# Kernel optimization log

Hardware: AMD Instinct MI355X
Metric: run time of the kernel (lower is better)

The kernel has to match this reference:

```python
import jax, jax.numpy as jnp
import numpy as np

B = 2048
NU, NF, NA = 20000, 100000, 20000  # users, feeds, authors
D = 150   # SVD embed dim for FM features
DK = 64   # tag/keyword/d2v embed dim


def setup_inputs() -> dict:
    key = jax.random.key(0)
    ks = jax.random.split(key, 24)
    r = lambda k, shape: (jax.random.normal(k, shape, dtype=jnp.float32) * 0.05)
    # ids: user, feed, author columns with their own vocab ranges
    u = jax.random.randint(ks[0], (B,), 0, NU)
    f = jax.random.randint(ks[1], (B,), 0, NF)
    a = jax.random.randint(ks[2], (B,), 0, NA)
    inputs = jnp.stack([u, f, a], axis=1).astype(jnp.int32)  # [B,3]
    first_order_shifts = jnp.array([0, NU, NU + NF], dtype=jnp.int32)
    return {
        'inputs': inputs,
        'first_order_shifts': first_order_shifts,
        'W_user_feed': r(ks[3], (NU, D)),
        'W_feed_user': r(ks[4], (NF, D)),
        'W_user_author': r(ks[5], (NU, D)),
        'W_author_user': r(ks[6], (NA, D)),
        'W_feed_emb': r(ks[7], (NF, D)),          # trainable=False in original
        'W_user_tag': r(ks[8], (NU, DK)),
        'W_user_key1': r(ks[9], (NU, DK)),
        'W_user_key2': r(ks[10], (NU, DK)),
        'W_feed_tag': r(ks[11], (NF, DK)),
        'W_feed_key1': r(ks[12], (NF, DK)),
        'W_feed_key2': r(ks[13], (NF, DK)),
        'W_uf_d2v': r(ks[14], (NU, DK)),
        'W_fu_d2v': r(ks[15], (NF, DK)),
        'W_ua_d2v': r(ks[16], (NU, DK)),
        'W_au_d2v': r(ks[17], (NA, DK)),
        'W256': r(ks[18], (2 * D * D, 256)),       # 45000 -> 256
        'b256': jnp.zeros((256,), jnp.float32),
        'W128': r(ks[19], (2 * DK * DK, 128)),     # 8192 -> 128
        'b128': jnp.zeros((128,), jnp.float32),
    }


def reference(inputs, first_order_shifts, W_user_feed, W_feed_user,
              W_user_author, W_author_user, W_feed_emb, W_user_tag,
              W_user_key1, W_user_key2, W_feed_tag, W_feed_key1, W_feed_key2,
              W_uf_d2v, W_fu_d2v, W_ua_d2v, W_au_d2v, W256, b256, W128, b128):
    inputs = inputs.reshape(-1, 3)
    u, f, a = inputs[:, 0], inputs[:, 1], inputs[:, 2]
    one_hot_inputs = inputs + first_order_shifts[None, :]

    user_feed_embed = W_user_feed[u]      # [B,150]
    user_author_embed = W_user_author[u]
    author_user_embed = W_author_user[a]
    feed_emb_embed = W_feed_emb[f]
    feed_user_embed = W_feed_user[f]
    user_tag_embed = W_user_tag[u]        # [B,64]
    user_key1_embed = W_user_key1[u]
    user_key2_embed = W_user_key2[u]
    feed_tag_embed = W_feed_tag[f]
    feed_key1_embed = W_feed_key1[f]
    feed_key2_embed = W_feed_key2[f]
    user_feed_d2vem = W_uf_d2v[u]
    user_author_d2vem = W_ua_d2v[u]
    feed_user_d2vem = W_fu_d2v[f]
    author_user_d2vem = W_au_d2v[a]

    # d2v outer products -> [B,64,64] each; concat axis=1 -> [B,128,64]
    user_w_feed = jnp.einsum('bi,bj->bij', user_feed_d2vem, feed_user_d2vem)
    user_w_auth = jnp.einsum('bi,bj->bij', user_author_d2vem, author_user_d2vem)
    user_w_user = jnp.concatenate([user_w_feed, user_w_auth], axis=1)
    user_w_user = user_w_user.reshape(-1, 2 * DK * DK)
    user_w_user = jax.nn.relu(user_w_user @ W128 + b128)  # Dropout inactive (inference)

    # SVD outer products -> [B,150,150] each; concat axis=1 -> [B,300,150]
    user_x_feed = jnp.einsum('bi,bj->bij', user_feed_embed, feed_user_embed)
    user_x_auth = jnp.einsum('bi,bj->bij', user_author_embed, author_user_embed)
    user_x_user = jnp.concatenate([user_x_feed, user_x_auth], axis=1)
    user_x_user = user_x_user.reshape(-1, 2 * D * D)
    user_x_user = jax.nn.relu(user_x_user @ W256 + b256)

    # tf.concat([list], axis=1) stacks the inner list -> [4,B,150], then reshape (-1,4,150)
    embeds_fm = jnp.stack([user_feed_embed, user_author_embed,
                           feed_user_embed, author_user_embed], axis=0)
    fm_embed_inputs = embeds_fm.reshape(-1, 4, D)

    expert_inputs = jnp.concatenate([
        user_feed_embed, user_author_embed, user_tag_embed, user_key1_embed,
        user_key2_embed, user_feed_d2vem, user_author_d2vem, feed_user_embed,
        feed_tag_embed, feed_key1_embed, feed_emb_embed, feed_key2_embed,
        feed_user_d2vem, author_user_embed, author_user_d2vem,
        user_x_user, user_w_user], axis=-1)  # [B,1710]
    return expert_inputs, one_hot_inputs, fm_embed_inputs
```

## Files before the change

### kernel.cpp

```cpp
#include <hip/hip_runtime.h>
#include <hip/hip_bf16.h>
#include <stdint.h>

#define BB   2048
#define DD   150
#define DKK  64

static constexpr int EXPERT_W  = 1774;
static constexpr int X_OFF     = 1390;
static constexpr int W_OFF     = 1646;
static constexpr int EXPERT_SZ = BB * EXPERT_W;
static constexpr int OH_BASE   = EXPERT_SZ;
static constexpr int FM_BASE   = OH_BASE + BB * 3;

static constexpr size_t WTX_OFF = 0;
static constexpr size_t WTW_OFF = 24576000;
static constexpr size_t WSX_OFF = 26673152;
static constexpr size_t WSW_OFF = 43450368;
static constexpr size_t WS_NEED = 51838976;

typedef __attribute__((ext_vector_type(8))) short bf16x8;
typedef __attribute__((ext_vector_type(4))) float f32x4;

union APack { int d[4]; bf16x8 v; };

__device__ __forceinline__ int cvtpk_bf16(float a, float b) {
  int r; asm("v_cvt_pk_bf16_f32 %0, %1, %2" : "=v"(r) : "v"(a), "v"(b)); return r;
}
__device__ __forceinline__ f32x4 mfma16(bf16x8 a, bf16x8 b, f32x4 c) {
  return __builtin_amdgcn_mfma_f32_16x16x32_bf16(a, b, c, 0, 0, 0);
}
__device__ __forceinline__ void gload16(const void* g, void* l) {
  __builtin_amdgcn_global_load_lds(
      (__attribute__((address_space(1))) void*)(g),
      (__attribute__((address_space(3))) void*)(l), 16, 0, 0);
}
__device__ __forceinline__ float bfu2f(uint32_t u) { return __uint_as_float(u << 16); }

__global__ __launch_bounds__(256) void prep_pack(
    const float* __restrict__ W256, __hip_bfloat16* __restrict__ WtX,
    const float* __restrict__ W128, __hip_bfloat16* __restrict__ WtW)
{
  const int blk = blockIdx.x;
  const int t = threadIdx.x;

  if (blk < 1500) {
    const int T  = blk;
    const int jj = T / 300;
    const int i  = T - jj*300;
    float v[32];
    const float* src = W256 + ((size_t)i*150 + jj*32)*256 + t;
    #pragma unroll
    for (int jl = 0; jl < 32; ++jl) {
      int j = jj*32 + jl;
      v[jl] = (j < 150) ? src[(size_t)jl*256] : 0.f;
    }
    const int b16 = t >> 4, nloc = t & 15;
    char* dst = (char*)WtX + (size_t)T*16384 + (size_t)(b16*512 + nloc*8)*2;
    #pragma unroll
    for (int ksub = 0; ksub < 4; ++ksub) {
      int pk0 = cvtpk_bf16(v[ksub*8+0], v[ksub*8+1]);
      int pk1 = cvtpk_bf16(v[ksub*8+2], v[ksub*8+3]);
      int pk2 = cvtpk_bf16(v[ksub*8+4], v[ksub*8+5]);
      int pk3 = cvtpk_bf16(v[ksub*8+6], v[ksub*8+7]);
      *(int4*)(dst + (size_t)ksub*256) = make_int4(pk0, pk1, pk2, pk3);
    }
  } else {
    if (t >= 128) return;
    const int T  = blk - 1500;
    const int jj = T >> 7;
    const int i  = T & 127;
    float v[32];
    const float* src = W128 + ((size_t)i*64 + jj*32)*128 + t;
    #pragma unroll
    for (int jl = 0; jl < 32; ++jl) v[jl] = src[(size_t)jl*128];
    const int b16 = t >> 4, nloc = t & 15;
    char* dst = (char*)WtW + (size_t)T*8192 + (size_t)(b16*512 + nloc*8)*2;
    #pragma unroll
    for (int ksub = 0; ksub < 4; ++ksub) {
      int pk0 = cvtpk_bf16(v[ksub*8+0], v[ksub*8+1]);
      int pk1 = cvtpk_bf16(v[ksub*8+2], v[ksub*8+3]);
      int pk2 = cvtpk_bf16(v[ksub*8+4], v[ksub*8+5]);
      int pk3 = cvtpk_bf16(v[ksub*8+6], v[ksub*8+7]);
      *(int4*)(dst + (size_t)ksub*256) = make_int4(pk0, pk1, pk2, pk3);
    }
  }
}

__global__ __launch_bounds__(512, 4) void mfma_fused(
    const int* __restrict__ inputs, const int* __restrict__ shifts,
    const float* __restrict__ Wuf, const float* __restrict__ Wua,
    const float* __restrict__ Wfu, const float* __restrict__ Wau,
    const float* __restrict__ Wfe,
    const float* __restrict__ Wut, const float* __restrict__ Wuk1, const float* __restrict__ Wuk2,
    const float* __restrict__ Wft, const float* __restrict__ Wfk1, const float* __restrict__ Wfk2,
    const float* __restrict__ Wufd, const float* __restrict__ Wuad,
    const float* __restrict__ Wfud, const float* __restrict__ Waud,
    const __hip_bfloat16* __restrict__ WtXt, __hip_bfloat16* __restrict__ wsX,
    const __hip_bfloat16* __restrict__ WtWt, __hip_bfloat16* __restrict__ wsW,
    float* __restrict__ out)
{
  __shared__ __align__(16) char smem[43008];
  const int tid = threadIdx.x;
  const int lane = tid & 63;
  const int w  = tid >> 6;
  const int lr = lane & 15;
  const int g  = lane >> 4;
  const unsigned wdst = (unsigned)(tid & ~63) * 16;

  if (blockIdx.x < 512) {
    float* xlds = (float*)smem;
    char*  bbase = smem + 10240;

    const int bid = blockIdx.x;
    const int h  = bid & 1;
    const int s  = (bid >> 1) & 15;
    const int mb = bid >> 5;
    const int b0 = mb * 128;
    const bool upper = s >= 8;
    const int sl  = upper ? s - 8 : s;
    const int i0l = sl * 19;
    const int cnt = (150 - i0l) < 19 ? (150 - i0l) : 19;
    const int ig0 = i0l + (upper ? 150 : 0);

    const float* X = upper ? Wua : Wuf;
    const float* Y = upper ? Wau : Wfu;
    const int yoff = upper ? 2 : 1;

    for (int k = tid; k < 128*20; k += 512) {
      int r = k / 20, ii = k - r*20;
      float v = 0.f;
      if (ii < cnt) v = X[(size_t)inputs[(b0+r)*3]*150 + i0l + ii];
      xlds[k] = v;
    }

    const int mg = w >> 1;
    const int ng = w & 1;

    int yid[2];
    #pragma unroll
    for (int mf = 0; mf < 2; ++mf)
      yid[mf] = inputs[(size_t)(b0 + mg*32 + mf*16 + lr)*3 + yoff];

    const char* wtb = (const char*)WtXt + (size_t)h*8192;

    int jjs = 0, iis = 0;
    auto stage1 = [&](int slot) {
      const char* sp = wtb + (size_t)(jjs*300 + ig0 + iis)*16384 + (size_t)tid*16;
      gload16(sp, bbase + (unsigned)slot*8192 + wdst);
      if (iis + 1 < cnt) ++iis;
      else if (jjs + 1 < 5) { iis = 0; ++jjs; }
    };

    f32x4 acc[2][4];
    #pragma unroll
    for (int i = 0; i < 2; ++i)
      #pragma unroll
      for (int j = 0; j < 4; ++j) acc[i][j] = (f32x4){0.f,0.f,0.f,0.f};

    const int NW = 5 * cnt;

    stage1(0); stage1(1); stage1(2);

    int jjc = 0, iic = 0;
    int yjj = -1;
    float yreg[2][8];

    for (int wi = 0; wi < NW; ++wi) {
      const int ahead = NW - 1 - wi;
      if (ahead >= 2)      asm volatile("s_waitcnt vmcnt(2)" ::: "memory");
      else if (ahead == 1) asm volatile("s_waitcnt vmcnt(1)" ::: "memory");
      else                 asm volatile("s_waitcnt vmcnt(0)" ::: "memory");
      __builtin_amdgcn_s_barrier();

      if (wi + 3 < NW) stage1((wi + 3) & 3);
      __builtin_amdgcn_sched_barrier(0);
      __builtin_amdgcn_s_setprio(1);

      if (jjc != yjj) {
        yjj = jjc;
        const int jb = jjc*32 + g*8;
        #pragma unroll
        for (int mf = 0; mf < 2; ++mf) {
          const float* yp = Y + (size_t)yid[mf]*150;
          if (jb + 8 <= 150) {
            #pragma unroll
            for (int hh = 0; hh < 4; ++hh) {
              float2 vv = *(const float2*)(yp + jb + 2*hh);
              yreg[mf][2*hh]   = vv.x;
              yreg[mf][2*hh+1] = vv.y;
            }
          } else {
            #pragma unroll
            for (int e = 0; e < 8; ++e)
              yreg[mf][e] = (jb + e < 150) ? yp[jb + e] : 0.f;
          }
        }
      }
      const __hip_bfloat16* bb = (const __hip_bfloat16*)(bbase + (unsigned)(wi & 3)*8192);
      bf16x8 bv[4];
      #pragma unroll
      for (int nf = 0; nf < 4; ++nf)
        bv[nf] = *(const bf16x8*)(bb + (ng*4 + nf)*512 + g*128 + lr*8);
      APack a[2];
      #pragma unroll
      for (int mf = 0; mf < 2; ++mf) {
        const float xv = xlds[(mg*32 + mf*16 + lr)*20 + iic];
        #pragma unroll
        for (int e = 0; e < 4; ++e)
          a[mf].d[e] = cvtpk_bf16(xv*yreg[mf][2*e], xv*yreg[mf][2*e+1]);
      }
      #pragma unroll
      for (int mf = 0; mf < 2; ++mf)
        #pragma unroll
        for (int nf = 0; nf < 4; ++nf)
          acc[mf][nf] = mfma16(a[mf].v, bv[nf], acc[mf][nf]);

      __builtin_amdgcn_s_setprio(0);
      ++iic; if (iic >= cnt) { iic = 0; ++jjc; }
    }

    __hip_bfloat16* wp = wsX + ((size_t)s*2048 + b0)*256;
    #pragma unroll
    for (int mf = 0; mf < 2; ++mf) {
      #pragma unroll
      for (int nf = 0; nf < 4; ++nf) {
        int rb  = mg*32 + mf*16 + g*4;
        int col = h*128 + ng*64 + nf*16 + lr;
        f32x4 v = acc[mf][nf];
        #pragma unroll
        for (int e = 0; e < 4; ++e)
          wp[(size_t)(rb+e)*256 + col] = __float2bfloat16(v[e]);
      }
    }

  } else if (blockIdx.x < 768) {
    float* xlds = (float*)smem;
    char*  bbase = smem + 4096;

    const int bidw = blockIdx.x - 512;
    const int mb = bidw >> 4;
    const int s  = bidw & 15;
    const int b0 = mb * 128;
    const bool upper = s >= 8;
    const int i0l = (s & 7) * 8;
    const int ig0 = i0l + (upper ? 64 : 0);

    const float* X = upper ? Wuad : Wufd;
    const float* Y = upper ? Waud : Wfud;
    const int yoff = upper ? 2 : 1;

    for (int k = tid; k < 128*8; k += 512) {
      int r = k >> 3, ii = k & 7;
      xlds[k] = X[(size_t)inputs[(size_t)(b0+r)*3]*64 + i0l + ii];
    }

    const int mg = w >> 1;
    const int ng = w & 1;

    int yid[2];
    #pragma unroll
    for (int mf = 0; mf < 2; ++mf)
      yid[mf] = inputs[(size_t)(b0 + mg*32 + mf*16 + lr)*3 + yoff];

    const char* wtb = (const char*)WtWt;

    auto stageT = [&](int bufi, int T) {
      const char* sp = wtb + (size_t)T*8192 + (size_t)tid*16;
      char* dp = bbase + (unsigned)bufi*16384 + wdst;
      gload16(sp,        dp);
      gload16(sp + 8192, dp + 8192);
    };

    f32x4 acc[2][4];
    #pragma unroll
    for (int i = 0; i < 2; ++i)
      #pragma unroll
      for (int j = 0; j < 4; ++j) acc[i][j] = (f32x4){0.f,0.f,0.f,0.f};

    stageT(0, ig0);
    stageT(1, ig0 + 2);

    int jjc = 0, iic = 0;
    int jjs = 0, iis = 4;
    int yjj = -1;
    float yreg[2][8];

    for (int p = 0; p < 8; ++p) {
      if (jjc != yjj) {
        yjj = jjc;
        const int jb = jjc*32 + g*8;
        #pragma unroll
        for (int mf = 0; mf < 2; ++mf) {
          const float* yp = Y + (size_t)yid[mf]*64 + jb;
          #pragma unroll
          for (int hh = 0; hh < 2; ++hh) {
            float4 v = *(const float4*)(yp + hh*4);
            yreg[mf][hh*4]   = v.x;
            yreg[mf][hh*4+1] = v.y;
            yreg[mf][hh*4+2] = v.z;
            yreg[mf][hh*4+3] = v.w;
          }
        }
      }
      if (p + 1 < 8) asm volatile("s_waitcnt vmcnt(2)" ::: "memory");
      else           asm volatile("s_waitcnt vmcnt(0)" ::: "memory");
      __builtin_amdgcn_s_barrier();
      __builtin_amdgcn_sched_barrier(0);

      const int buf = p & 1;
      #pragma unroll
      for (int sc = 0; sc < 2; ++sc) {
        const __hip_bfloat16* bb = (const __hip_bfloat16*)(bbase + (unsigned)buf*16384 + (unsigned)sc*8192);
        bf16x8 bv[4];
        #pragma unroll
        for (int nf = 0; nf < 4; ++nf)
          bv[nf] = *(const bf16x8*)(bb + (ng*4 + nf)*512 + g*128 + lr*8);
        APack a[2];
        #pragma unroll
        for (int mf = 0; mf < 2; ++mf) {
          float xv = xlds[(mg*32 + mf*16 + lr)*8 + iic + sc];
          #pragma unroll
          for (int e = 0; e < 4; ++e)
            a[mf].d[e] = cvtpk_bf16(xv*yreg[mf][2*e], xv*yreg[mf][2*e+1]);
        }
        #pragma unroll
        for (int mf = 0; mf < 2; ++mf)
          #pragma unroll
          for (int nf = 0; nf < 4; ++nf)
            acc[mf][nf] = mfma16(a[mf].v, bv[nf], acc[mf][nf]);
      }

      __builtin_amdgcn_s_barrier();
      if (p + 2 < 8) stageT(buf, jjs*128 + ig0 + iis);

      iic += 2; if (iic >= 8) { iic = 0; ++jjc; }
      iis += 2; if (iis >= 8) { iis = 0; ++jjs; }
    }

    __hip_bfloat16* wp = wsW + ((size_t)s*2048 + b0)*128;
    #pragma unroll
    for (int mf = 0; mf < 2; ++mf) {
      #pragma unroll
      for (int nf = 0; nf < 4; ++nf) {
        int rb  = mg*32 + mf*16 + g*4;
        int col = ng*64 + nf*16 + lr;
        f32x4 v = acc[mf][nf];
        #pragma unroll
        for (int e = 0; e < 4; ++e)
          wp[(size_t)(rb+e)*128 + col] = __float2bfloat16(v[e]);
      }
    }

  } else {
    const int b = blockIdx.x - 768;
    const int u = inputs[b*3 + 0];
    const int f = inputs[b*3 + 1];
    const int a = inputs[b*3 + 2];
    float* row = out + b * EXPERT_W;
    float* fm  = out + FM_BASE;
    const int t = tid;

    for (int c = t; c < DD; c += 512) {
        float ufe = Wuf[u*DD + c];
        float uae = Wua[u*DD + c];
        float fue = Wfu[f*DD + c];
        float fee = Wfe[f*DD + c];
        float aue = Wau[a*DD + c];
        row[0    + c] = ufe;
        row[150  + c] = uae;
        row[620  + c] = fue;
        row[898  + c] = fee;
        row[1176 + c] = aue;
        fm[0*BB*DD + b*DD + c] = ufe;
        fm[1*BB*DD + b*DD + c] = uae;
        fm[2*BB*DD + b*DD + c] = fue;
        fm[3*BB*DD + b*DD + c] = aue;
    }
    for (int c = t; c < DKK; c += 512) {
        row[300  + c] = Wut [u*DKK + c];
        row[364  + c] = Wuk1[u*DKK + c];
        row[428  + c] = Wuk2[u*DKK + c];
        row[492  + c] = Wufd[u*DKK + c];
        row[556  + c] = Wuad[u*DKK + c];
        row[770  + c] = Wft [f*DKK + c];
        row[834  + c] = Wfk1[f*DKK + c];
        row[1048 + c] = Wfk2[f*DKK + c];
        row[1112 + c] = Wfud[f*DKK + c];
        row[1326 + c] = Waud[a*DKK + c];
    }
    if (t < 3) out[OH_BASE + b*3 + t] = (float)(inputs[b*3 + t] + shifts[t]);
  }
}

__global__ __launch_bounds__(256) void epilogue_kernel(
    const __hip_bfloat16* __restrict__ wsX, const __hip_bfloat16* __restrict__ wsW,
    const float* __restrict__ b256, const float* __restrict__ b128,
    float* __restrict__ out)
{
  int idx = blockIdx.x*256 + threadIdx.x;
  if (idx >= BB*192) return;
  int b = idx / 192, c2 = idx - b*192;
  if (c2 < 128) {
    int c = c2*2;
    float a0 = b256[c], a1 = b256[c+1];
    #pragma unroll
    for (int k = 0; k < 16; ++k) {
      uint32_t u = *(const uint32_t*)(wsX + ((size_t)k*BB + b)*256 + c);
      a0 += bfu2f(u);
      a1 += __uint_as_float(u & 0xffff0000u);
    }
    float2 r = make_float2(a0 > 0.f ? a0 : 0.f, a1 > 0.f ? a1 : 0.f);
    *(float2*)(out + (size_t)b*EXPERT_W + X_OFF + c) = r;
  } else {
    int cc = (c2 - 128)*2;
    float a0 = b128[cc], a1 = b128[cc+1];
    #pragma unroll
    for (int k = 0; k < 16; ++k) {
      uint32_t u = *(const uint32_t*)(wsW + ((size_t)k*BB + b)*128 + cc);
      a0 += bfu2f(u);
      a1 += __uint_as_float(u & 0xffff0000u);
    }
    float2 r = make_float2(a0 > 0.f ? a0 : 0.f, a1 > 0.f ? a1 : 0.f);
    *(float2*)(out + (size_t)b*EXPERT_W + W_OFF + cc) = r;
  }
}

__global__ __launch_bounds__(256) void gather_kernel(
    const int* __restrict__ inputs, const int* __restrict__ shifts,
    const float* __restrict__ Wuf, const float* __restrict__ Wfu,
    const float* __restrict__ Wua, const float* __restrict__ Wau,
    const float* __restrict__ Wfe,
    const float* __restrict__ Wut, const float* __restrict__ Wuk1, const float* __restrict__ Wuk2,
    const float* __restrict__ Wft, const float* __restrict__ Wfk1, const float* __restrict__ Wfk2,
    const float* __restrict__ Wufd, const float* __restrict__ Wfud,
    const float* __restrict__ Wuad, const float* __restrict__ Waud,
    float* __restrict__ out)
{
    const int b = blockIdx.x;
    const int u = inputs[b*3 + 0];
    const int f = inputs[b*3 + 1];
    const int a = inputs[b*3 + 2];
    float* row = out + b * EXPERT_W;
    float* fm  = out + FM_BASE;
    const int t = threadIdx.x;

    for (int c = t; c < DD; c += 256) {
        float ufe = Wuf[u*DD + c];
        float uae = Wua[u*DD + c];
        float fue = Wfu[f*DD + c];
        float fee = Wfe[f*DD + c];
        float aue = Wau[a*DD + c];
        row[0    + c] = ufe;
        row[150  + c] = uae;
        row[620  + c] = fue;
        row[898  + c] = fee;
        row[1176 + c] = aue;
        fm[0*BB*DD + b*DD + c] = ufe;
        fm[1*BB*DD + b*DD + c] = uae;
        fm[2*BB*DD + b*DD + c] = fue;
        fm[3*BB*DD + b*DD + c] = aue;
    }
    for (int c = t; c < DKK; c += 256) {
        row[300  + c] = Wut [u*DKK + c];
        row[364  + c] = Wuk1[u*DKK + c];
        row[428  + c] = Wuk2[u*DKK + c];
        row[492  + c] = Wufd[u*DKK + c];
        row[556  + c] = Wuad[u*DKK + c];
        row[770  + c] = Wft [f*DKK + c];
        row[834  + c] = Wfk1[f*DKK + c];
        row[1048 + c] = Wfk2[f*DKK + c];
        row[1112 + c] = Wfud[f*DKK + c];
        row[1326 + c] = Waud[a*DKK + c];
    }
    if (t < 3) {
        out[OH_BASE + b*3 + t] = (float)(inputs[b*3 + t] + shifts[t]);
    }
}

static constexpr int NPAIR_X = 300 * 150;
static constexpr int CHX     = 128;

__global__ __launch_bounds__(256) void xuser_kernel(
    const int* __restrict__ inputs,
    const float* __restrict__ Wuf, const float* __restrict__ Wua,
    const float* __restrict__ Wfu, const float* __restrict__ Wau,
    const float* __restrict__ W256, const float* __restrict__ b256,
    float* __restrict__ out)
{
    __shared__ float xs[16][308];
    __shared__ float ys[16][308];
    __shared__ float xy[CHX][16];
    const int half = blockIdx.x & 1;
    const int bg   = blockIdx.x >> 1;
    const int b0   = bg * 16;
    const int t    = threadIdx.x;
    const int bl   = t & 15;
    const int kg   = t >> 4;
    const int kbase = half * 128 + kg * 8;
    for (int idx = t; idx < 16 * DD; idx += 256) {
        int bb = idx / DD;
        int c  = idx - bb * DD;
        int u = inputs[(b0+bb)*3 + 0];
        int f = inputs[(b0+bb)*3 + 1];
        int a = inputs[(b0+bb)*3 + 2];
        xs[bb][c]       = Wuf[u*DD + c];
        xs[bb][150 + c] = Wua[u*DD + c];
        ys[bb][c]       = Wfu[f*DD + c];
        ys[bb][150 + c] = Wau[a*DD + c];
    }
    float acc[8] = {0,0,0,0,0,0,0,0};
    for (int base = 0; base < NPAIR_X; base += CHX) {
        __syncthreads();
        #pragma unroll
        for (int r = 0; r < (CHX*16)/256; ++r) {
            int idx = t + r * 256;
            int pl  = idx >> 4;
            int bb  = idx & 15;
            int p   = base + pl;
            if (p < NPAIR_X) {
                int i = p / 150;
                int j = p - i * 150;
                xy[pl][bb] = xs[bb][i] * ys[bb][(i >= 150 ? 150 : 0) + j];
            }
        }
        __syncthreads();
        const int lim = min(CHX, NPAIR_X - base);
        const float* wp = W256 + base * 256 + kbase;
        for (int pl = 0; pl < lim; ++pl) {
            float sv = xy[pl][bl];
            const float4* w4 = (const float4*)(wp + pl * 256);
            float4 w0 = w4[0], w1 = w4[1];
            acc[0] = fmaf(sv, w0.x, acc[0]); acc[1] = fmaf(sv, w0.y, acc[1]);
            acc[2] = fmaf(sv, w0.z, acc[2]); acc[3] = fmaf(sv, w0.w, acc[3]);
            acc[4] = fmaf(sv, w1.x, acc[4]); acc[5] = fmaf(sv, w1.y, acc[5]);
            acc[6] = fmaf(sv, w1.z, acc[6]); acc[7] = fmaf(sv, w1.w, acc[7]);
        }
    }
    const int rowbase = (b0 + bl) * EXPERT_W + X_OFF;
    #pragma unroll
    for (int m = 0; m < 8; ++m) {
        float v = acc[m] + b256[kbase + m];
        out[rowbase + kbase + m] = (v > 0.f ? v : 0.f);
    }
}

static constexpr int NPAIR_W = 128 * 64;
static constexpr int CHW     = 256;

__global__ __launch_bounds__(256) void wuser_kernel(
    const int* __restrict__ inputs,
    const float* __restrict__ Wufd, const float* __restrict__ Wuad,
    const float* __restrict__ Wfud, const float* __restrict__ Waud,
    const float* __restrict__ W128, const float* __restrict__ b128,
    float* __restrict__ out)
{
    __shared__ float xs[8][132];
    __shared__ float ys[8][132];
    __shared__ float xy[CHW][8];
    const int bg = blockIdx.x;
    const int b0 = bg * 8;
    const int t  = threadIdx.x;
    const int bl = t & 7;
    const int kg = t >> 3;
    const int kbase = kg * 4;
    for (int idx = t; idx < 8 * DKK; idx += 256) {
        int bb = idx >> 6;
        int c  = idx & 63;
        int u = inputs[(b0+bb)*3 + 0];
        int f = inputs[(b0+bb)*3 + 1];
        int a = inputs[(b0+bb)*3 + 2];
        xs[bb][c]      = Wufd[u*DKK + c];
        xs[bb][64 + c] = Wuad[u*DKK + c];
        ys[bb][c]      = Wfud[f*DKK + c];
        ys[bb][64 + c] = Waud[a*DKK + c];
    }
    float acc[4] = {0,0,0,0};
    for (int base = 0; base < NPAIR_W; base += CHW) {
        __syncthreads();
        #pragma unroll
        for (int r = 0; r < (CHW*8)/256; ++r) {
            int idx = t + r * 256;
            int pl  = idx >> 3;
            int bb  = idx & 7;
            int p   = base + pl;
            int i = p >> 6;
            int j = p & 63;
            xy[pl][bb] = xs[bb][i] * ys[bb][(i >= 64 ? 64 : 0) + j];
        }
        __syncthreads();
        const float* wp = W128 + base * 128 + kbase;
        for (int pl = 0; pl < CHW; ++pl) {
            float sv = xy[pl][bl];
            float4 wv = *(const float4*)(wp + pl * 128);
            acc[0] = fmaf(sv, wv.x, acc[0]); acc[1] = fmaf(sv, wv.y, acc[1]);
            acc[2] = fmaf(sv, wv.z, acc[2]); acc[3] = fmaf(sv, wv.w, acc[3]);
        }
    }
    const int rowbase = (b0 + bl) * EXPERT_W + W_OFF;
    #pragma unroll
    for (int m = 0; m < 4; ++m) {
        float v = acc[m] + b128[kbase + m];
        out[rowbase + kbase + m] = (v > 0.f ? v : 0.f);
    }
}

extern "C" void kernel_launch(void* const* d_in, const int* in_sizes, int n_in,
                              void* d_out, int out_size, void* d_ws, size_t ws_size,
                              hipStream_t stream)
{
    const int*   inputs = (const int*)  d_in[0];
    const int*   shifts = (const int*)  d_in[1];
    const float* Wuf    = (const float*)d_in[2];
    const float* Wfu    = (const float*)d_in[3];
    const float* Wua    = (const float*)d_in[4];
    const float* Wau    = (const float*)d_in[5];
    const float* Wfe    = (const float*)d_in[6];
    const float* Wut    = (const float*)d_in[7];
    const float* Wuk1   = (const float*)d_in[8];
    const float* Wuk2   = (const float*)d_in[9];
    const float* Wft    = (const float*)d_in[10];
    const float* Wfk1   = (const float*)d_in[11];
    const float* Wfk2   = (const float*)d_in[12];
    const float* Wufd   = (const float*)d_in[13];
    const float* Wfud   = (const float*)d_in[14];
    const float* Wuad   = (const float*)d_in[15];
    const float* Waud   = (const float*)d_in[16];
    const float* W256   = (const float*)d_in[17];
    const float* b256   = (const float*)d_in[18];
    const float* W128   = (const float*)d_in[19];
    const float* b128   = (const float*)d_in[20];

    float* out = (float*)d_out;

    if (ws_size >= WS_NEED) {
        char* ws = (char*)d_ws;
        __hip_bfloat16* WtX = (__hip_bfloat16*)(ws + WTX_OFF);
        __hip_bfloat16* WtW = (__hip_bfloat16*)(ws + WTW_OFF);
        __hip_bfloat16* wsX = (__hip_bfloat16*)(ws + WSX_OFF);
        __hip_bfloat16* wsW = (__hip_bfloat16*)(ws + WSW_OFF);

        prep_pack<<<1756, 256, 0, stream>>>(W256, WtX, W128, WtW);

        mfma_fused<<<2816, 512, 0, stream>>>(inputs, shifts,
            Wuf, Wua, Wfu, Wau, Wfe, Wut, Wuk1, Wuk2, Wft, Wfk1, Wfk2,
            Wufd, Wuad, Wfud, Waud,
            WtX, wsX, WtW, wsW, out);

        epilogue_kernel<<<(BB*192 + 255)/256, 256, 0, stream>>>(wsX, wsW, b256, b128, out);
    } else {
        gather_kernel<<<BB, 256, 0, stream>>>(inputs, shifts,
            Wuf, Wfu, Wua, Wau, Wfe, Wut, Wuk1, Wuk2, Wft, Wfk1, Wfk2,
            Wufd, Wfud, Wuad, Waud, out);
        xuser_kernel<<<256, 256, 0, stream>>>(inputs, Wuf, Wua, Wfu, Wau, W256, b256, out);
        wuser_kernel<<<256, 256, 0, stream>>>(inputs, Wufd, Wuad, Wfud, Waud, W128, b128, out);
    }
}
```

Baseline: 97.95 us.

## Move gather rows into prep kernel and shrink MFMA pipeline to three stages

The per-row embedding gather and copy blocks move out of the MFMA kernel and into the weight-packing prep kernel, so the MFMA launch holds only GEMM blocks. The MFMA staging ring drops from four 8 KB buffers to three, which cuts LDS per block and lets launch bounds allow 8 blocks per CU instead of 4. The aim is higher occupancy for the GEMM and letting the gather overlap with weight packing. The cost is a shallower prefetch (two loads in flight instead of three), which may expose more global-load latency.

```diff
diff --git a/kernel.cpp b/kernel.cpp
--- a/kernel.cpp
+++ b/kernel.cpp
@@ -37,15 +37,62 @@
 }
 __device__ __forceinline__ float bfu2f(uint32_t u) { return __uint_as_float(u << 16); }
 
-__global__ __launch_bounds__(256) void prep_pack(
+__global__ __launch_bounds__(256) void prep_kernel(
+    const int* __restrict__ inputs, const int* __restrict__ shifts,
+    const float* __restrict__ Wuf, const float* __restrict__ Wfu,
+    const float* __restrict__ Wua, const float* __restrict__ Wau,
+    const float* __restrict__ Wfe,
+    const float* __restrict__ Wut, const float* __restrict__ Wuk1, const float* __restrict__ Wuk2,
+    const float* __restrict__ Wft, const float* __restrict__ Wfk1, const float* __restrict__ Wfk2,
+    const float* __restrict__ Wufd, const float* __restrict__ Wfud,
+    const float* __restrict__ Wuad, const float* __restrict__ Waud,
     const float* __restrict__ W256, __hip_bfloat16* __restrict__ WtX,
-    const float* __restrict__ W128, __hip_bfloat16* __restrict__ WtW)
+    const float* __restrict__ W128, __hip_bfloat16* __restrict__ WtW,
+    float* __restrict__ out)
 {
   const int blk = blockIdx.x;
   const int t = threadIdx.x;
 
-  if (blk < 1500) {
-    const int T  = blk;
+  if (blk < 2048) {
+    const int b = blk;
+    const int u = inputs[b*3 + 0];
+    const int f = inputs[b*3 + 1];
+    const int a = inputs[b*3 + 2];
+    float* row = out + b * EXPERT_W;
+    float* fm  = out + FM_BASE;
+
+    for (int c = t; c < DD; c += 256) {
+        float ufe = Wuf[u*DD + c];
+        float uae = Wua[u*DD + c];
+        float fue = Wfu[f*DD + c];
+        float fee = Wfe[f*DD + c];
+        float aue = Wau[a*DD + c];
+        row[0    + c] = ufe;
+        row[150  + c] = uae;
+        row[620  + c] = fue;
+        row[898  + c] = fee;
+        row[1176 + c] = aue;
+        fm[0*BB*DD + b*DD + c] = ufe;
+        fm[1*BB*DD + b*DD + c] = uae;
+        fm[2*BB*DD + b*DD + c] = fue;
+        fm[3*BB*DD + b*DD + c] = aue;
+    }
+    for (int c = t; c < DKK; c += 256) {
+        row[300  + c] = Wut [u*DKK + c];
+        row[364  + c] = Wuk1[u*DKK + c];
+        row[428  + c] = Wuk2[u*DKK + c];
+        row[492  + c] = Wufd[u*DKK + c];
+        row[556  + c] = Wuad[u*DKK + c];
+        row[770  + c] = Wft [f*DKK + c];
+        row[834  + c] = Wfk1[f*DKK + c];
+        row[1048 + c] = Wfk2[f*DKK + c];
+        row[1112 + c] = Wfud[f*DKK + c];
+        row[1326 + c] = Waud[a*DKK + c];
+    }
+    if (t < 3) out[OH_BASE + b*3 + t] = (float)(inputs[b*3 + t] + shifts[t]);
+
+  } else if (blk < 2048 + 1500) {
+    const int T  = blk - 2048;
     const int jj = T / 300;
     const int i  = T - jj*300;
     float v[32];
@@ -65,9 +112,10 @@
       int pk3 = cvtpk_bf16(v[ksub*8+6], v[ksub*8+7]);
       *(int4*)(dst + (size_t)ksub*256) = make_int4(pk0, pk1, pk2, pk3);
     }
+
   } else {
     if (t >= 128) return;
-    const int T  = blk - 1500;
+    const int T  = blk - 3548;
     const int jj = T >> 7;
     const int i  = T & 127;
     float v[32];
@@ -87,20 +135,16 @@
   }
 }
 
-__global__ __launch_bounds__(512, 4) void mfma_fused(
-    const int* __restrict__ inputs, const int* __restrict__ shifts,
+__global__ __launch_bounds__(512, 8) void mfma_fused(
+    const int* __restrict__ inputs,
     const float* __restrict__ Wuf, const float* __restrict__ Wua,
     const float* __restrict__ Wfu, const float* __restrict__ Wau,
-    const float* __restrict__ Wfe,
-    const float* __restrict__ Wut, const float* __restrict__ Wuk1, const float* __restrict__ Wuk2,
-    const float* __restrict__ Wft, const float* __restrict__ Wfk1, const float* __restrict__ Wfk2,
     const float* __restrict__ Wufd, const float* __restrict__ Wuad,
     const float* __restrict__ Wfud, const float* __restrict__ Waud,
     const __hip_bfloat16* __restrict__ WtXt, __hip_bfloat16* __restrict__ wsX,
-    const __hip_bfloat16* __restrict__ WtWt, __hip_bfloat16* __restrict__ wsW,
-    float* __restrict__ out)
+    const __hip_bfloat16* __restrict__ WtWt, __hip_bfloat16* __restrict__ wsW)
 {
-  __shared__ __align__(16) char smem[43008];
+  __shared__ __align__(16) char smem[36864];
   const int tid = threadIdx.x;
   const int lane = tid & 63;
   const int w  = tid >> 6;
@@ -160,20 +204,20 @@
 
     const int NW = 5 * cnt;
 
-    stage1(0); stage1(1); stage1(2);
+    stage1(0); stage1(1);
 
     int jjc = 0, iic = 0;
+    int scons = 0, sstage = 2;
     int yjj = -1;
     float yreg[2][8];
 
     for (int wi = 0; wi < NW; ++wi) {
       const int ahead = NW - 1 - wi;
-      if (ahead >= 2)      asm volatile("s_waitcnt vmcnt(2)" ::: "memory");
-      else if (ahead == 1) asm volatile("s_waitcnt vmcnt(1)" ::: "memory");
-      else                 asm volatile("s_waitcnt vmcnt(0)" ::: "memory");
+      if (ahead >= 1) asm volatile("s_waitcnt vmcnt(1)" ::: "memory");
+      else            asm volatile("s_waitcnt vmcnt(0)" ::: "memory");
       __builtin_amdgcn_s_barrier();
 
-      if (wi + 3 < NW) stage1((wi + 3) & 3);
+      if (wi + 2 < NW) stage1(sstage);
       __builtin_amdgcn_sched_barrier(0);
       __builtin_amdgcn_s_setprio(1);
 
@@ -197,7 +241,7 @@
           }
         }
       }
-      const __hip_bfloat16* bb = (const __hip_bfloat16*)(bbase + (unsigned)(wi & 3)*8192);
+      const __hip_bfloat16* bb = (const __hip_bfloat16*)(bbase + (unsigned)scons*8192);
       bf16x8 bv[4];
       #pragma unroll
       for (int nf = 0; nf < 4; ++nf)
@@ -218,6 +262,8 @@
 
       __builtin_amdgcn_s_setprio(0);
       ++iic; if (iic >= cnt) { iic = 0; ++jjc; }
+      ++scons;  if (scons  == 3) scons  = 0;
+      ++sstage; if (sstage == 3) sstage = 0;
     }
 
     __hip_bfloat16* wp = wsX + ((size_t)s*2048 + b0)*256;
@@ -234,7 +280,7 @@
       }
     }
 
-  } else if (blockIdx.x < 768) {
+  } else {
     float* xlds = (float*)smem;
     char*  bbase = smem + 4096;
 
@@ -351,45 +397,6 @@
           wp[(size_t)(rb+e)*128 + col] = __float2bfloat16(v[e]);
       }
     }
-
-  } else {
-    const int b = blockIdx.x - 768;
-    const int u = inputs[b*3 + 0];
-    const int f = inputs[b*3 + 1];
-    const int a = inputs[b*3 + 2];
-    float* row = out + b * EXPERT_W;
-    float* fm  = out + FM_BASE;
-    const int t = tid;
-
-    for (int c = t; c < DD; c += 512) {
-        float ufe = Wuf[u*DD + c];
-        float uae = Wua[u*DD + c];
-        float fue = Wfu[f*DD + c];
-        float fee = Wfe[f*DD + c];
-        float aue = Wau[a*DD + c];
-        row[0    + c] = ufe;
-        row[150  + c] = uae;
-        row[620  + c] = fue;
-        row[898  + c] = fee;
-        row[1176 + c] = aue;
-        fm[0*BB*DD + b*DD + c] = ufe;
-        fm[1*BB*DD + b*DD + c] = uae;
-        fm[2*BB*DD + b*DD + c] = fue;
-        fm[3*BB*DD + b*DD + c] = aue;
-    }
-    for (int c = t; c < DKK; c += 512) {
-        row[300  + c] = Wut [u*DKK + c];
-        row[364  + c] = Wuk1[u*DKK + c];
-        row[428  + c] = Wuk2[u*DKK + c];
-        row[492  + c] = Wufd[u*DKK + c];
-        row[556  + c] = Wuad[u*DKK + c];
-        row[770  + c] = Wft [f*DKK + c];
-        row[834  + c] = Wfk1[f*DKK + c];
-        row[1048 + c] = Wfk2[f*DKK + c];
-        row[1112 + c] = Wfud[f*DKK + c];
-        row[1326 + c] = Waud[a*DKK + c];
-    }
-    if (t < 3) out[OH_BASE + b*3 + t] = (float)(inputs[b*3 + t] + shifts[t]);
   }
 }
 
@@ -640,12 +647,13 @@
         __hip_bfloat16* wsX = (__hip_bfloat16*)(ws + WSX_OFF);
         __hip_bfloat16* wsW = (__hip_bfloat16*)(ws + WSW_OFF);
 
-        prep_pack<<<1756, 256, 0, stream>>>(W256, WtX, W128, WtW);
-
-        mfma_fused<<<2816, 512, 0, stream>>>(inputs, shifts,
-            Wuf, Wua, Wfu, Wau, Wfe, Wut, Wuk1, Wuk2, Wft, Wfk1, Wfk2,
-            Wufd, Wuad, Wfud, Waud,
-            WtX, wsX, WtW, wsW, out);
+        prep_kernel<<<3804, 256, 0, stream>>>(inputs, shifts,
+            Wuf, Wfu, Wua, Wau, Wfe, Wut, Wuk1, Wuk2, Wft, Wfk1, Wfk2,
+            Wufd, Wfud, Wuad, Waud, W256, WtX, W128, WtW, out);
+
+        mfma_fused<<<768, 512, 0, stream>>>(inputs,
+            Wuf, Wua, Wfu, Wau, Wufd, Wuad, Wfud, Waud,
+            WtX, wsX, WtW, wsW);
 
         epilogue_kernel<<<(BB*192 + 255)/256, 256, 0, stream>>>(wsX, wsW, b256, b128, out);
     } else {
```

After: 308.2 us. +214.6%, slower.
